# Kernel tuning notes

Measured on AMD Instinct MI355X. Metric: run time of the kernel, lower is better.

Reference implementation:

```python
import jax, jax.numpy as jnp
import numpy as np

GAMMA = 1.0        # soft-min temperature for differentiable DTW
BIG = 1e9          # value for cells outside the Sakoe-Chiba band
DTW_BW = 0.2       # band width as fraction of normalized path deviation
AVG_T_LEN = True   # divide discrepancy by input sequence length


def _softmin3(a, b, c):
    # differentiable min over the three DP predecessors
    z = jnp.stack([a, b, c], axis=0)
    return -GAMMA * jax.nn.logsumexp(-z / GAMMA, axis=0)


def _dtw(C, mask):
    """Band-limited soft-DTW DP. C: [T,K] pairwise costs, mask: [T,K] bool band.
    Returns scalar D[T-1,K-1]. Row scan over T; inner scan over K carries the
    left neighbor (recurrence D[i,j] = C[i,j] + softmin(D[i-1,j], D[i,j-1], D[i-1,j-1]))."""
    T, K = C.shape

    def row_step(carry, inp):
        prev_row, diag0 = carry            # prev_row: D[i-1,:]; diag0: virtual D[i-1,-1]
        c_row, m_row = inp
        diag = jnp.concatenate([diag0[None], prev_row[:-1]])  # D[i-1,j-1]

        def col_step(left, xs):
            c, up, dg, m = xs
            d = c + _softmin3(up, left, dg)
            d = jnp.where(m, d, BIG)       # kill cells outside the band
            return d, d

        _, row = jax.lax.scan(col_step, jnp.float32(BIG), (c_row, prev_row, diag, m_row))
        return (row, jnp.float32(BIG)), None

    # virtual border: D[-1,-1] = 0, all other border cells = BIG
    init = (jnp.full((K,), BIG, dtype=jnp.float32), jnp.float32(0.0))
    (last_row, _), _ = jax.lax.scan(row_step, init, (C, mask))
    return last_row[-1]


def setup_inputs() -> dict:
    key = jax.random.key(0)
    kx, kp = jax.random.split(key)
    B, T = 64, 512
    F, K = 32, 64
    x = jax.random.normal(kx, (B, T), dtype=jnp.float32)
    protos = jax.random.normal(kp, (F, K), dtype=jnp.float32)  # learnable DTW kernels
    return {"x": x, "protos": protos}


def reference(x, protos):
    B, T = x.shape
    F, K = protos.shape
    # pairwise squared costs: [B, F, T, K]
    C = (x[:, None, :, None] - protos[None, :, None, :]) ** 2
    # Sakoe-Chiba band on normalized coordinates
    ii = jnp.arange(T, dtype=jnp.float32) / (T - 1)
    jj = jnp.arange(K, dtype=jnp.float32) / (K - 1)
    mask = jnp.abs(ii[:, None] - jj[None, :]) <= DTW_BW  # [T, K]
    d = jax.vmap(jax.vmap(lambda c: _dtw(c, mask)))(C)    # [B, F]
    if AVG_T_LEN:
        d = d / jnp.float32(T)
    return d[:, :, None]  # [B, num_filter, out_len=1]
```

## Files before the change

kernel.cpp:

```cpp
#include <hip/hip_runtime.h>

#define T_LEN  512
#define K_LEN  64
#define NFILT  32
#define NBATCH 64
#define XOFS   64
#define XS_SZ  640
#define CHUNK  32
#define SQRT_LOG2E 1.2011224087864498f
#define LN2        0.6931471805599453f

static __device__ __forceinline__ float wave_shr1(float x) {
    int r = __builtin_amdgcn_update_dpp(0, __builtin_bit_cast(int, x),
                                        0x138, 0xF, 0xF, true);
    return __builtin_bit_cast(float, r);
}

template <int N>
static __device__ __forceinline__ float row_ror(float x) {
    int r = __builtin_amdgcn_update_dpp(0, __builtin_bit_cast(int, x),
                                        0x120 + N, 0xF, 0xF, true);
    return __builtin_bit_cast(float, r);
}

static __device__ __forceinline__ float exp2_fast(float x) {
#if __has_builtin(__builtin_amdgcn_exp2f)
    return __builtin_amdgcn_exp2f(x);
#else
    return exp2f(x);
#endif
}

__global__ __launch_bounds__(256) void dtw_kernel(const float* __restrict__ x,
                                                  const float* __restrict__ protos,
                                                  float* __restrict__ out) {
    __shared__ float xs[XS_SZ];
    const int tid  = threadIdx.x;
    const int lane = tid & 63;
    const int wid  = tid >> 6;
    const int b    = blockIdx.x >> 3;
    const int f    = ((blockIdx.x & 7) << 2) | wid;

    for (int t0 = tid; t0 < XS_SZ; t0 += 256) {
        int i = t0 - XOFS;
        xs[t0] = (i >= 0 && i < T_LEN) ? x[b * T_LEN + i] * SQRT_LOG2E : 0.0f;
    }
    __syncthreads();

    const float p  = protos[f * K_LEN + lane] * SQRT_LOG2E;
    const float jj = (float)lane / 63.0f;

    int a0 = 0, b0 = T_LEN - 1;
    while (a0 < b0) { int m = (a0 + b0) >> 1;
        if ((float)m / 511.0f - jj >= -0.2f) b0 = m; else a0 = m + 1; }
    const int ilo = a0;
    a0 = 0; b0 = T_LEN - 1;
    while (a0 < b0) { int m = (a0 + b0 + 1) >> 1;
        if ((float)m / 511.0f - jj <= 0.2f) a0 = m; else b0 = m - 1; }
    const int ihi = a0;

    const unsigned range = (unsigned)(ihi - ilo);
    unsigned t = (unsigned)(-(lane + ilo));
    float prev = 0.0f;
    float dgp  = (lane == 0) ? 1.0f : 0.0f;
    int   S2   = 0;
    int   base = XOFS - lane;

    float A[CHUNK], B[CHUNK];
#pragma unroll
    for (int k = 0; k < CHUNK; ++k) A[k] = xs[base + k];

#define STEP(XV) do {                                   \
        float df_   = (XV) - p;                         \
        float w_    = exp2_fast(-(df_ * df_));          \
        w_          = (t <= range) ? w_ : 0.0f;         \
        float a_    = prev + dgp;        \
        float left_ = wave_shr1(prev);                  \
        dgp  = left_;                                   \
        prev = (a_ + left_) * w_;                       \
        ++t;                                            \
    } while (0)

#define RENORM() do {                                                        \
        float m_ = prev;                                                     \
        m_ = fmaxf(m_, row_ror<8>(m_));                                      \
        m_ = fmaxf(m_, row_ror<4>(m_));                                      \
        m_ = fmaxf(m_, row_ror<2>(m_));                                      \
        m_ = fmaxf(m_, row_ror<1>(m_));                                      \
        int mi_ = __builtin_bit_cast(int, m_);                               \
        unsigned r0_ = (unsigned)__builtin_amdgcn_readlane(mi_, 0);          \
        unsigned r1_ = (unsigned)__builtin_amdgcn_readlane(mi_, 16);         \
        unsigned r2_ = (unsigned)__builtin_amdgcn_readlane(mi_, 32);         \
        unsigned r3_ = (unsigned)__builtin_amdgcn_readlane(mi_, 48);         \
        unsigned ra_ = r0_ > r1_ ? r0_ : r1_;                                \
        unsigned rb_ = r2_ > r3_ ? r2_ : r3_;                                \
        unsigned mx_ = ra_ > rb_ ? ra_ : rb_;                                \
        int e_  = (int)((mx_ >> 23) & 0xFF);                                 \
        int Me_ = 284 - e_;                                                  \
        Me_ = Me_ < 1 ? 1 : (Me_ > 254 ? 254 : Me_);                         \
        float M_ = __builtin_bit_cast(float, Me_ << 23);                     \
        S2  += Me_ - 127;                                                    \
        prev *= M_;                                                          \
        dgp  *= M_;                                                          \
    } while (0)

#pragma unroll 1
    for (int cc = 0; cc < 8; ++cc) {
#pragma unroll
        for (int k = 0; k < CHUNK; ++k) B[k] = xs[base + CHUNK + k];
#pragma unroll
        for (int k = 0; k < CHUNK; ++k) STEP(A[k]);
        RENORM();
        base += CHUNK;
#pragma unroll
        for (int k = 0; k < CHUNK; ++k) A[k] = xs[base + CHUNK + k];
#pragma unroll
        for (int k = 0; k < CHUNK; ++k) STEP(B[k]);
        RENORM();
        base += CHUNK;
    }
#pragma unroll
    for (int k = 0; k < CHUNK; ++k) B[k] = xs[base + CHUNK + k];
#pragma unroll
    for (int k = 0; k < CHUNK; ++k) STEP(A[k]);
    RENORM();
#pragma unroll
    for (int k = 0; k < 31; ++k) STEP(B[k]);

    if (lane == 63) {
        float D = ((float)S2 - log2f(prev)) * LN2;
        out[b * NFILT + f] = D * (1.0f / (float)T_LEN);
    }
#undef STEP
#undef RENORM
}

extern "C" void kernel_launch(void* const* d_in, const int* in_sizes, int n_in,
                              void* d_out, int out_size, void* d_ws, size_t ws_size,
                              hipStream_t stream) {
    const float* x      = (const float*)d_in[0];
    const float* protos = (const float*)d_in[1];
    float* out          = (float*)d_out;

    dim3 grid(NBATCH * (NFILT / 4));
    dim3 block(256);
    hipLaunchKernelGGL(dtw_kernel, grid, block, 0, stream, x, protos, out);
}
```

Baseline: 31.14 us.

## Stream x through wave lanes via DPP shift and software-pipeline exp weights

Drops the shared-memory staging of x. Each x value is now injected at lane 0 and passed down the wave with a DPP right shift, so lane j sees x[i-j] without LDS reads or a block barrier. The exp2 weight computation runs two steps ahead of the dependent DP update (double-buffered w0/w1), taking the exp latency off the serial recurrence chain. The mask is folded into the exp2 argument as a large negative offset. In exchange there are extra DPP shifts per step, more wave-uniform global loads of x, and a longer tail loop.

```diff
diff --git a/kernel.cpp b/kernel.cpp
--- a/kernel.cpp
+++ b/kernel.cpp
@@ -4,9 +4,6 @@
 #define K_LEN  64
 #define NFILT  32
 #define NBATCH 64
-#define XOFS   64
-#define XS_SZ  640
-#define CHUNK  32
 #define SQRT_LOG2E 1.2011224087864498f
 #define LN2        0.6931471805599453f
 
@@ -34,21 +31,17 @@
 __global__ __launch_bounds__(256) void dtw_kernel(const float* __restrict__ x,
                                                   const float* __restrict__ protos,
                                                   float* __restrict__ out) {
-    __shared__ float xs[XS_SZ];
     const int tid  = threadIdx.x;
     const int lane = tid & 63;
     const int wid  = tid >> 6;
-    const int b    = blockIdx.x >> 3;
-    const int f    = ((blockIdx.x & 7) << 2) | wid;
+    const int idx  = (blockIdx.x << 2) | wid;
+    const int b    = idx >> 5;
+    const int f    = idx & 31;
 
-    for (int t0 = tid; t0 < XS_SZ; t0 += 256) {
-        int i = t0 - XOFS;
-        xs[t0] = (i >= 0 && i < T_LEN) ? x[b * T_LEN + i] * SQRT_LOG2E : 0.0f;
-    }
-    __syncthreads();
-
-    const float p  = protos[f * K_LEN + lane] * SQRT_LOG2E;
+    const float* __restrict__ xr = x + b * T_LEN;
+    const float pn = -protos[f * K_LEN + lane] * SQRT_LOG2E;
     const float jj = (float)lane / 63.0f;
+    const bool lane0 = (lane == 0);
 
     int a0 = 0, b0 = T_LEN - 1;
     while (a0 < b0) { int m = (a0 + b0) >> 1;
@@ -61,24 +54,34 @@
 
     const unsigned range = (unsigned)(ihi - ilo);
     unsigned t = (unsigned)(-(lane + ilo));
-    float prev = 0.0f;
-    float dgp  = (lane == 0) ? 1.0f : 0.0f;
-    int   S2   = 0;
-    int   base = XOFS - lane;
+    float xv = 0.0f, prev = 0.0f;
+    float dgp = lane0 ? 1.0f : 0.0f;
+    int   S2  = 0;
+    float w0, w1;
 
-    float A[CHUNK], B[CHUNK];
-#pragma unroll
-    for (int k = 0; k < CHUNK; ++k) A[k] = xs[base + k];
+#define LEAD_COMMON(W) do {                                     \
+        float sel_ = (t <= range) ? 0.0f : -3.0e38f;            \
+        ++t;                                                    \
+        float ds_  = __builtin_fmaf(xv, SQRT_LOG2E, pn);        \
+        W = exp2_fast(__builtin_fmaf(ds_, -ds_, sel_));         \
+    } while (0)
 
-#define STEP(XV) do {                                   \
-        float df_   = (XV) - p;                         \
-        float w_    = exp2_fast(-(df_ * df_));          \
-        w_          = (t <= range) ? w_ : 0.0f;         \
-        float a_    = prev + dgp;        \
-        float left_ = wave_shr1(prev);                  \
-        dgp  = left_;                                   \
-        prev = (a_ + left_) * w_;                       \
-        ++t;                                            \
+#define LEAD_INJ(W, SV) do {                                    \
+        float xs_ = wave_shr1(xv);                              \
+        xv = lane0 ? (SV) : xs_;                                \
+        LEAD_COMMON(W);                                         \
+    } while (0)
+
+#define LEAD_NOINJ(W) do {                                      \
+        xv = wave_shr1(xv);     \
+        LEAD_COMMON(W);                                         \
+    } while (0)
+
+#define CONSUME(W) do {                                         \
+        float l_ = wave_shr1(prev);                             \
+        float a_ = prev + dgp;                                  \
+        dgp  = l_;                                              \
+        prev = (a_ + l_) * (W);                                 \
     } while (0)
 
 #define RENORM() do {                                                        \
@@ -104,34 +107,73 @@
         dgp  *= M_;                                                          \
     } while (0)
 
+    float SA[32], SB[32];
+#pragma unroll
+    for (int k = 0; k < 32; ++k) SA[k] = xr[k];
+
+    LEAD_INJ(w0, SA[0]);
+    LEAD_INJ(w1, SA[1]);
+
 #pragma unroll 1
-    for (int cc = 0; cc < 8; ++cc) {
+    for (int c = 0; c < 7; ++c) {
+        const int o1 = (2 * c + 1) * 32;
 #pragma unroll
-        for (int k = 0; k < CHUNK; ++k) B[k] = xs[base + CHUNK + k];
+        for (int k = 0; k < 32; ++k) SB[k] = xr[o1 + k];
 #pragma unroll
-        for (int k = 0; k < CHUNK; ++k) STEP(A[k]);
+        for (int k = 0; k < 32; ++k) {
+            float sv = (k <= 29) ? SA[k + 2] : SB[k - 30];
+            if (k & 1) { CONSUME(w1); LEAD_INJ(w1, sv); }
+            else       { CONSUME(w0); LEAD_INJ(w0, sv); }
+        }
         RENORM();
-        base += CHUNK;
+        const int o2 = (2 * c + 2) * 32;
 #pragma unroll
-        for (int k = 0; k < CHUNK; ++k) A[k] = xs[base + CHUNK + k];
+        for (int k = 0; k < 32; ++k) SA[k] = xr[o2 + k];
 #pragma unroll
-        for (int k = 0; k < CHUNK; ++k) STEP(B[k]);
+        for (int k = 0; k < 32; ++k) {
+            float sv = (k <= 29) ? SB[k + 2] : SA[k - 30];
+            if (k & 1) { CONSUME(w1); LEAD_INJ(w1, sv); }
+            else       { CONSUME(w0); LEAD_INJ(w0, sv); }
+        }
         RENORM();
-        base += CHUNK;
     }
 #pragma unroll
-    for (int k = 0; k < CHUNK; ++k) B[k] = xs[base + CHUNK + k];
+    for (int k = 0; k < 32; ++k) SB[k] = xr[15 * 32 + k];
 #pragma unroll
-    for (int k = 0; k < CHUNK; ++k) STEP(A[k]);
+    for (int k = 0; k < 32; ++k) {
+        float sv = (k <= 29) ? SA[k + 2] : SB[k - 30];
+        if (k & 1) { CONSUME(w1); LEAD_INJ(w1, sv); }
+        else       { CONSUME(w0); LEAD_INJ(w0, sv); }
+    }
     RENORM();
 #pragma unroll
-    for (int k = 0; k < 31; ++k) STEP(B[k]);
+    for (int k = 0; k < 32; ++k) {
+        if (k & 1) { CONSUME(w1); if (k <= 29) LEAD_INJ(w1, SB[k + 2]); else LEAD_NOINJ(w1); }
+        else       { CONSUME(w0); if (k <= 29) LEAD_INJ(w0, SB[k + 2]); else LEAD_NOINJ(w0); }
+    }
+    RENORM();
+#pragma unroll
+    for (int k = 0; k < 32; ++k) {
+        if (k & 1) { CONSUME(w1); LEAD_NOINJ(w1); }
+        else       { CONSUME(w0); LEAD_NOINJ(w0); }
+    }
+    RENORM();
+#pragma unroll
+    for (int k = 0; k < 29; ++k) {
+        if (k & 1) { CONSUME(w1); LEAD_NOINJ(w1); }
+        else       { CONSUME(w0); LEAD_NOINJ(w0); }
+    }
+    CONSUME(w1);
+    CONSUME(w0);
 
     if (lane == 63) {
         float D = ((float)S2 - log2f(prev)) * LN2;
         out[b * NFILT + f] = D * (1.0f / (float)T_LEN);
     }
-#undef STEP
+#undef LEAD_COMMON
+#undef LEAD_INJ
+#undef LEAD_NOINJ
+#undef CONSUME
 #undef RENORM
 }
 
@@ -142,7 +184,7 @@
     const float* protos = (const float*)d_in[1];
     float* out          = (float*)d_out;
 
-    dim3 grid(NBATCH * (NFILT / 4));
+    dim3 grid(512);
     dim3 block(256);
     hipLaunchKernelGGL(dtw_kernel, grid, block, 0, stream, x, protos, out);
 }
```

Result: slower. 36.85 us (+18.3%).

## Split each soft-DTW into forward and backward half-passes joined at midpoint

Applied to the files above, without the earlier changes.

Each (batch, filter) DTW is now computed by two wavefronts. One runs the forward recurrence over the first half of the time axis, the other runs the reversed recurrence from the end over the second half. Their boundary values are combined through LDS with a sum over adjacent column pairs to form the total path weight. This roughly halves the serial dependency chain per problem and doubles the wavefront count, at the cost of a boundary capture, an extra rescale and an LDS exchange. Correctness depends on the midpoint join covering every path exactly once.

```diff
diff --git a/kernel.cpp b/kernel.cpp
--- a/kernel.cpp
+++ b/kernel.cpp
@@ -3,10 +3,8 @@
 #define T_LEN  512
 #define K_LEN  64
 #define NFILT  32
-#define NBATCH 64
 #define XOFS   64
-#define XS_SZ  640
-#define CHUNK  32
+#define XS_SZ  384
 #define SQRT_LOG2E 1.2011224087864498f
 #define LN2        0.6931471805599453f
 
@@ -31,58 +29,81 @@
 #endif
 }
 
-__global__ __launch_bounds__(256) void dtw_kernel(const float* __restrict__ x,
-                                                  const float* __restrict__ protos,
-                                                  float* __restrict__ out) {
-    __shared__ float xs[XS_SZ];
+static __device__ __forceinline__ void band_iv(float jj, int& lo, int& hi) {
+    int a0 = 0, b0 = T_LEN - 1;
+    while (a0 < b0) { int m = (a0 + b0) >> 1;
+        if ((float)m / 511.0f - jj >= -0.2f) b0 = m; else a0 = m + 1; }
+    lo = a0;
+    a0 = 0; b0 = T_LEN - 1;
+    while (a0 < b0) { int m = (a0 + b0 + 1) >> 1;
+        if ((float)m / 511.0f - jj <= 0.2f) a0 = m; else b0 = m - 1; }
+    hi = a0;
+}
+
+__global__ __launch_bounds__(128, 4) void dtw_kernel(const float* __restrict__ x,
+                                                     const float* __restrict__ protos,
+                                                     float* __restrict__ out) {
+    __shared__ float xsF[XS_SZ];
+    __shared__ float xsB[XS_SZ];
+    __shared__ float capB_lds[65];
+    __shared__ int   s2B_lds;
     const int tid  = threadIdx.x;
     const int lane = tid & 63;
     const int wid  = tid >> 6;
-    const int b    = blockIdx.x >> 3;
-    const int f    = ((blockIdx.x & 7) << 2) | wid;
+    const int b    = blockIdx.x >> 5;
+    const int f    = blockIdx.x & 31;
 
-    for (int t0 = tid; t0 < XS_SZ; t0 += 256) {
+    for (int t0 = tid; t0 < XS_SZ; t0 += 128) {
         int i = t0 - XOFS;
-        xs[t0] = (i >= 0 && i < T_LEN) ? x[b * T_LEN + i] * SQRT_LOG2E : 0.0f;
+        bool ok = (i >= 0);
+        xsF[t0] = ok ? x[b * T_LEN + i] * SQRT_LOG2E : 0.0f;
+        xsB[t0] = ok ? x[b * T_LEN + (T_LEN - 1) - i] * SQRT_LOG2E : 0.0f;
     }
     __syncthreads();
 
-    const float p  = protos[f * K_LEN + lane] * SQRT_LOG2E;
-    const float jj = (float)lane / 63.0f;
+    const int col = wid ? (63 - lane) : lane;
+    const float pn = -protos[f * K_LEN + col] * SQRT_LOG2E;
 
-    int a0 = 0, b0 = T_LEN - 1;
-    while (a0 < b0) { int m = (a0 + b0) >> 1;
-        if ((float)m / 511.0f - jj >= -0.2f) b0 = m; else a0 = m + 1; }
-    const int ilo = a0;
-    a0 = 0; b0 = T_LEN - 1;
-    while (a0 < b0) { int m = (a0 + b0 + 1) >> 1;
-        if ((float)m / 511.0f - jj <= 0.2f) a0 = m; else b0 = m - 1; }
-    const int ihi = a0;
+    int ilo, ihi;
+    band_iv((float)col / 63.0f, ilo, ihi);
+    int lo, hi;
+    if (wid == 0) { lo = ilo; hi = (ihi < 255) ? ihi : 255; }
+    else {
+        int loBo = (ilo > 256) ? ilo : 256;
+        lo = (T_LEN - 1) - ihi;
+        hi = (T_LEN - 1) - loBo;
+    }
+    unsigned t, range;
+    if (lo > hi) { t = 0x80000000u; range = 0u; }
+    else { t = (unsigned)(-(lane + lo)); range = (unsigned)(hi - lo); }
 
-    const unsigned range = (unsigned)(ihi - ilo);
-    unsigned t = (unsigned)(-(lane + ilo));
-    float prev = 0.0f;
+    float prev = 0.0f, cap = 0.0f;
     float dgp  = (lane == 0) ? 1.0f : 0.0f;
     int   S2   = 0;
-    int   base = XOFS - lane;
+    const int dcap = 255 + lane;
+    const float* __restrict__ xp = (wid ? xsB : xsF) + (XOFS - lane);
 
-    float A[CHUNK], B[CHUNK];
+    float A[32], Bv[32];
 #pragma unroll
-    for (int k = 0; k < CHUNK; ++k) A[k] = xs[base + k];
+    for (int k = 0; k < 32; ++k) A[k] = xp[k];
+    __builtin_amdgcn_sched_barrier(0);
 
-#define STEP(XV) do {                                   \
-        float df_   = (XV) - p;                         \
-        float w_    = exp2_fast(-(df_ * df_));          \
-        w_          = (t <= range) ? w_ : 0.0f;         \
-        float a_    = prev + dgp;        \
-        float left_ = wave_shr1(prev);                  \
-        dgp  = left_;                                   \
-        prev = (a_ + left_) * w_;                       \
-        ++t;                                            \
+#define STEP(XV, DCONST, CAPF) do {                           \
+        float xv_  = (XV);                                    \
+        float sel_ = (t <= range) ? 0.0f : -3.0e38f;          \
+        ++t;                                                  \
+        float d_ = xv_ + pn;                                  \
+        float w_ = exp2_fast(__builtin_fmaf(d_, -d_, sel_));  \
+        float l_ = wave_shr1(prev);                           \
+        float a_ = prev + dgp;                                \
+        float s_ = a_ + l_;                                   \
+        dgp  = l_;                                            \
+        prev = s_ * w_;                                       \
+        if (CAPF) cap = (dcap == (DCONST)) ? prev : cap;      \
     } while (0)
 
-#define RENORM() do {                                                        \
-        float m_ = prev;                                                     \
+#define RESCALE(VAL, TGT, APPLY) do {                                        \
+        float m_ = VAL;                                                      \
         m_ = fmaxf(m_, row_ror<8>(m_));                                      \
         m_ = fmaxf(m_, row_ror<4>(m_));                                      \
         m_ = fmaxf(m_, row_ror<2>(m_));                                      \
@@ -96,43 +117,68 @@
         unsigned rb_ = r2_ > r3_ ? r2_ : r3_;                                \
         unsigned mx_ = ra_ > rb_ ? ra_ : rb_;                                \
         int e_  = (int)((mx_ >> 23) & 0xFF);                                 \
-        int Me_ = 284 - e_;                                                  \
+        int Me_ = (TGT) - e_;                                                \
         Me_ = Me_ < 1 ? 1 : (Me_ > 254 ? 254 : Me_);                         \
         float M_ = __builtin_bit_cast(float, Me_ << 23);                     \
-        S2  += Me_ - 127;                                                    \
-        prev *= M_;                                                          \
-        dgp  *= M_;                                                          \
+        S2 += Me_ - 127;                                                     \
+        APPLY;                                                               \
     } while (0)
 
-#pragma unroll 1
-    for (int cc = 0; cc < 8; ++cc) {
+#define RENORM() RESCALE(prev, 284, { prev *= M_; dgp *= M_; cap *= M_; })
+
+#define CHUNKRUN(CBASE, CUR, NXT, CAPF) do {                                 \
+        _Pragma("unroll")                                                    \
+        for (int k = 0; k < 32; ++k) NXT[k] = xp[(CBASE) + 32 + k];          \
+        __builtin_amdgcn_sched_barrier(0);                                   \
+        _Pragma("unroll")                                                    \
+        for (int k = 0; k < 32; ++k) STEP(CUR[k], (CBASE) + k, CAPF);        \
+        RENORM();                                                            \
+        __builtin_amdgcn_sched_barrier(0);                                   \
+    } while (0)
+
+    CHUNKRUN(  0, A,  Bv, 0);
+    CHUNKRUN( 32, Bv, A,  0);
+    CHUNKRUN( 64, A,  Bv, 0);
+    CHUNKRUN( 96, Bv, A,  0);
+    CHUNKRUN(128, A,  Bv, 0);
+    CHUNKRUN(160, Bv, A,  0);
+    CHUNKRUN(192, A,  Bv, 0);
+    CHUNKRUN(224, Bv, A,  1);
+    CHUNKRUN(256, A,  Bv, 1);
 #pragma unroll
-        for (int k = 0; k < CHUNK; ++k) B[k] = xs[base + CHUNK + k];
-#pragma unroll
-        for (int k = 0; k < CHUNK; ++k) STEP(A[k]);
-        RENORM();
-        base += CHUNK;
-#pragma unroll
-        for (int k = 0; k < CHUNK; ++k) A[k] = xs[base + CHUNK + k];
-#pragma unroll
-        for (int k = 0; k < CHUNK; ++k) STEP(B[k]);
-        RENORM();
-        base += CHUNK;
+    for (int k = 0; k < 31; ++k) STEP(Bv[k], 288 + k, 1);
+
+    RESCALE(cap, 254, { cap *= M_; });
+
+    if (wid == 1) {
+        capB_lds[63 - lane] = cap;
+        if (lane == 0) { capB_lds[64] = 0.0f; s2B_lds = S2; }
     }
-#pragma unroll
-    for (int k = 0; k < CHUNK; ++k) B[k] = xs[base + CHUNK + k];
-#pragma unroll
-    for (int k = 0; k < CHUNK; ++k) STEP(A[k]);
-    RENORM();
-#pragma unroll
-    for (int k = 0; k < 31; ++k) STEP(B[k]);
+    __syncthreads();
 
-    if (lane == 63) {
-        float D = ((float)S2 - log2f(prev)) * LN2;
-        out[b * NFILT + f] = D * (1.0f / (float)T_LEN);
+    if (wid == 0) {
+        float cb0 = capB_lds[lane];
+        float cb1 = capB_lds[lane + 1];
+        float s = cap * (cb0 + cb1);
+        float m = s;
+        m += row_ror<8>(m);
+        m += row_ror<4>(m);
+        m += row_ror<2>(m);
+        m += row_ror<1>(m);
+        int mi = __builtin_bit_cast(int, m);
+        float tot = m;
+        tot += __builtin_bit_cast(float, __builtin_amdgcn_readlane(mi, 0));
+        tot += __builtin_bit_cast(float, __builtin_amdgcn_readlane(mi, 16));
+        tot += __builtin_bit_cast(float, __builtin_amdgcn_readlane(mi, 32));
+        if (lane == 63) {
+            float D = ((float)(S2 + s2B_lds) - log2f(tot)) * LN2;
+            out[b * NFILT + f] = D * (1.0f / (float)T_LEN);
+        }
     }
 #undef STEP
+#undef RESCALE
 #undef RENORM
+#undef CHUNKRUN
 }
 
 extern "C" void kernel_launch(void* const* d_in, const int* in_sizes, int n_in,
@@ -142,7 +188,7 @@
     const float* protos = (const float*)d_in[1];
     float* out          = (float*)d_out;
 
-    dim3 grid(NBATCH * (NFILT / 4));
-    dim3 block(256);
+    dim3 grid(64 * 32);
+    dim3 block(128);
     hipLaunchKernelGGL(dtw_kernel, grid, block, 0, stream, x, protos, out);
 }
```

After: 36.22 us. +16.3%, slower.
